# Optimization experiments

Measured on AMD Instinct MI355X. Metric: run time of the kernel, lower is better.

The kernel has to match this reference:

```python
import jax, jax.numpy as jnp
import numpy as np

N, T, F_IN, H, D_FF, C_OUT = 4096, 60, 64, 128, 256, 1


def _gru_layer(x_tnf, W_ih, W_hh, b_ih, b_hh):
    # torch nn.GRU single layer; x_tnf: [T, N, in]
    def step(h, xt):
        gi = xt @ W_ih.T + b_ih          # [N, 3H]
        gh = h @ W_hh.T + b_hh
        i_r, i_z, i_n = jnp.split(gi, 3, axis=-1)
        h_r, h_z, h_n = jnp.split(gh, 3, axis=-1)
        r = jax.nn.sigmoid(i_r + h_r)
        z = jax.nn.sigmoid(i_z + h_z)
        n = jnp.tanh(i_n + r * h_n)
        h = (1.0 - z) * n + z * h
        return h, h
    h0 = jnp.zeros((x_tnf.shape[1], W_hh.shape[1]), x_tnf.dtype)
    hT, ys = jax.lax.scan(step, h0, x_tnf)
    return hT, ys


def setup_inputs() -> dict:
    key = jax.random.key(0)
    ks = jax.random.split(key, 20)
    s_in = 1.0 / np.sqrt(F_IN)
    s_h = 1.0 / np.sqrt(H)
    inp = {
        'x': jax.random.normal(ks[0], (N, T, F_IN), jnp.float32),
        'W_ih0': jax.random.normal(ks[1], (3 * H, F_IN), jnp.float32) * s_in,
        'W_hh0': jax.random.normal(ks[2], (3 * H, H), jnp.float32) * s_h,
        'b_ih0': jax.random.normal(ks[3], (3 * H,), jnp.float32) * s_h,
        'b_hh0': jax.random.normal(ks[4], (3 * H,), jnp.float32) * s_h,
        'W_ih1': jax.random.normal(ks[5], (3 * H, H), jnp.float32) * s_h,
        'W_hh1': jax.random.normal(ks[6], (3 * H, H), jnp.float32) * s_h,
        'b_ih1': jax.random.normal(ks[7], (3 * H,), jnp.float32) * s_h,
        'b_hh1': jax.random.normal(ks[8], (3 * H,), jnp.float32) * s_h,
        'Wt': jax.random.normal(ks[9], (H, H), jnp.float32) * s_h,
        'bt': jax.random.normal(ks[10], (H,), jnp.float32) * s_h,
        'a': jax.random.normal(ks[11], (2 * H, 1), jnp.float32),
        'Wfc': jax.random.normal(ks[12], (H, H), jnp.float32) * s_h,
        'bfc': jax.random.normal(ks[13], (H,), jnp.float32) * s_h,
        'Wp1': jax.random.normal(ks[14], (D_FF, H), jnp.float32) * s_h,
        'bp1': jax.random.normal(ks[15], (D_FF,), jnp.float32) * s_h,
        'Wp2': jax.random.normal(ks[16], (C_OUT, D_FF), jnp.float32) * (1.0 / np.sqrt(D_FF)),
        'bp2': jax.random.normal(ks[17], (C_OUT,), jnp.float32) * (1.0 / np.sqrt(D_FF)),
    }
    return inp


def reference(x, W_ih0, W_hh0, b_ih0, b_hh0, W_ih1, W_hh1, b_ih1, b_hh1,
              Wt, bt, a, Wfc, bfc, Wp1, bp1, Wp2, bp2):
    x_tnf = jnp.transpose(x, (1, 0, 2))  # [T, N, F]
    _, ys0 = _gru_layer(x_tnf, W_ih0, W_hh0, b_ih0, b_hh0)
    hT, _ = _gru_layer(ys0, W_ih1, W_hh1, b_ih1, b_hh1)
    hidden = hT  # out[:, -1, :], [N, H]

    # cal_attention: score[i,j] = a[:H].x_j + a[H:].x_i  (separable GAT score)
    xt = hidden @ Wt.T + bt                      # transformation(x) == transformation(y)
    a_flat = a[:, 0]
    s_j = xt @ a_flat[:H]                        # [N], contributes per-column
    s_i = xt @ a_flat[H:]                        # [N], contributes per-row
    scores = jax.nn.leaky_relu(s_i[:, None] + s_j[None, :], negative_slope=0.01)
    att = jax.nn.softmax(scores, axis=1)         # [N, N]

    hidden = att @ hidden + hidden
    hidden = jax.nn.leaky_relu(hidden @ Wfc.T + bfc, negative_slope=0.01)
    h1 = jax.nn.gelu(hidden @ Wp1.T + bp1, approximate=False)
    out = h1 @ Wp2.T + bp2                       # [N, 1]
    return jnp.squeeze(out)                      # [N]
```

## Files before the change

kernel.cpp:

```cpp
#include <hip/hip_runtime.h>
#include <cstdint>
#include <cstddef>

#define TSTEPS 60
#define NB 4096
#define HD 128

typedef __attribute__((ext_vector_type(8))) short short8;
typedef __attribute__((ext_vector_type(4))) float f32x4;

#define WS_SJ    0
#define WS_SI    16384
#define WS_HID   32768
#define WS_HTH   2129920
#define WS_HTL   3178496
#define WS_F0H   4227072
#define WS_F0L   (WS_F0H+49152)
#define WS_FR0H  (WS_F0L+49152)
#define WS_FR0L  (WS_FR0H+98304)
#define WS_FR1H  (WS_FR0L+98304)
#define WS_FR1L  (WS_FR1H+98304)
#define WS_FR2H  (WS_FR1L+98304)
#define WS_FR2L  (WS_FR2H+98304)
#define WS_BASE  (WS_FR2L+98304)
#define WS_Y0P   WS_BASE
#define WS_FULL  (WS_Y0P + 125829120ULL)


__device__ __forceinline__ float b2f(unsigned short h){ return __uint_as_float(((unsigned)h)<<16); }
__device__ __forceinline__ unsigned short f2b(float f){
  unsigned u = __float_as_uint(f);
  u = (u + 0x7FFFu + ((u>>16)&1u)) >> 16;
  return (unsigned short)u;
}
__device__ __forceinline__ float sigm(float x){ return 1.0f/(1.0f + __expf(-x)); }
__device__ __forceinline__ float tanhfast(float x){
  float xc = fminf(fmaxf(x,-15.0f),15.0f);
  float e = __expf(2.0f*xc);
  return (e-1.0f)/(e+1.0f);
}
__device__ __forceinline__ float lrelu(float x){ return x > 0.0f ? x : 0.01f*x; }
__device__ __forceinline__ float ldr1(const void* p, size_t i, int f32){
  return f32 ? ((const float*)p)[i] : b2f(((const unsigned short*)p)[i]);
}
template<bool F32>
__device__ __forceinline__ float4 ldg4c(const void* p, size_t i){
  if (F32) return *(const float4*)((const float*)p + i);
  ushort4 u = *(const ushort4*)((const unsigned short*)p + i);
  float4 f; f.x=b2f(u.x); f.y=b2f(u.y); f.z=b2f(u.z); f.w=b2f(u.w); return f;
}
__device__ __forceinline__ f32x4 f4zero(){ f32x4 v = {0.f,0.f,0.f,0.f}; return v; }
__device__ __forceinline__ void pinv(short8& v){ asm volatile("" : "+v"(v)); }

__device__ __forceinline__ void ldsbar(){
  asm volatile("s_waitcnt lgkmcnt(0)\n\ts_barrier" ::: "memory");
}

__device__ int probe_f32(const void* p, int nprobe, volatile int* s){
  if (threadIdx.x == 0) *s = 0;
  __syncthreads();
  if ((int)threadIdx.x < nprobe) {
    float v = b2f(((const unsigned short*)p)[threadIdx.x]);
    if (!(v == v) || fabsf(v) > 1e4f) *s = 1;
  }
  __syncthreads();
  int r = *s;
  __syncthreads();
  return r;
}

__global__ void diag_kernel(float* out, float code){
  int i = blockIdx.x*256 + threadIdx.x;
  if (i < 4096) out[i] = code;
}

__device__ void repack_mat(const void* src, int f32, int K, int nks,
                           unsigned short* hi, unsigned short* lo,
                           int tid, int nthr){
  int total = 384*K;
  for (int idx = tid; idx < total; idx += nthr) {
    int j = idx & 7, lane = (idx>>3)&63, t = idx>>9;
    int ks = t % nks, g = (t/nks)%3, w = t/(nks*3);
    int row = 16*(w + 8*g) + (lane & 15);
    int k   = ks*32 + ((lane>>4)<<3) + j;
    float v = f32 ? ((const float*)src)[(size_t)row*K + k]
                  : b2f(((const unsigned short*)src)[(size_t)row*K + k]);
    unsigned short h = f2b(v);
    hi[idx] = h;
    lo[idx] = f2b(v - b2f(h));
  }
}

__global__ __launch_bounds__(256) void repack_kernel(
    const void* wih0, const void* whh0, const void* wih1, const void* whh1,
    char* ws)
{
  __shared__ int sp;
  int f0 = probe_f32(wih0, 256, &sp);
  int f1 = probe_f32(whh0, 256, &sp);
  int f2 = probe_f32(wih1, 256, &sp);
  int f3 = probe_f32(whh1, 256, &sp);
  int tid  = blockIdx.x*256 + threadIdx.x;
  int nthr = gridDim.x*256;
  repack_mat(wih0, f0,  64, 2, (unsigned short*)(ws+WS_F0H),  (unsigned short*)(ws+WS_F0L),  tid, nthr);
  repack_mat(whh0, f1, 128, 4, (unsigned short*)(ws+WS_FR0H), (unsigned short*)(ws+WS_FR0L), tid, nthr);
  repack_mat(wih1, f2, 128, 4, (unsigned short*)(ws+WS_FR1H), (unsigned short*)(ws+WS_FR1L), tid, nthr);
  repack_mat(whh1, f3, 128, 4, (unsigned short*)(ws+WS_FR2H), (unsigned short*)(ws+WS_FR2L), tid, nthr);
}

#define MFMA __builtin_amdgcn_mfma_f32_16x16x32_bf16

__global__ __launch_bounds__(1024)
void gru0_kernel(const void* __restrict__ xg,
                 const void* __restrict__ bih0, const void* __restrict__ bhh0,
                 const char* __restrict__ ws, unsigned* __restrict__ y0p)
{
  __shared__ __align__(16) unsigned short xbh[2][1152], xbl[2][1152];
  __shared__ __align__(16) unsigned short hbh[2][2176], hbl[2][2176];
  __shared__ __align__(16) float pex[8192];
  __shared__ int sp;
  const int tid  = threadIdx.x;
  const int W    = tid >> 6;
  const int cg   = W >> 1;
  const int kh   = W & 1;
  const int lane = tid & 63;
  const int ln   = lane & 15;
  const int kq   = lane >> 4;
  const int r0   = blockIdx.x * 16;

  int xf  = probe_f32(xg,   256, &sp);
  int fb0 = probe_f32(bih0, 256, &sp);
  int fh0 = probe_f32(bhh0, 256, &sp);

  const unsigned short* f0h  = (const unsigned short*)(ws+WS_F0H);
  const unsigned short* f0l  = (const unsigned short*)(ws+WS_F0L);
  const unsigned short* fr0h = (const unsigned short*)(ws+WS_FR0H);
  const unsigned short* fr0l = (const unsigned short*)(ws+WS_FR0L);

  short8 X0h[3], X0l[3];
  #pragma unroll
  for (int g = 0; g < 3; ++g) {
    int fi = (cg*3+g)*2 + kh;
    X0h[g] = *(const short8*)&f0h[fi*512 + lane*8];
    X0l[g] = *(const short8*)&f0l[fi*512 + lane*8];
    pinv(X0h[g]); pinv(X0l[g]);
  }
  short8 R0h[3][2], R0l[3][2];
  #pragma unroll
  for (int g = 0; g < 3; ++g)
    #pragma unroll
    for (int jj = 0; jj < 2; ++jj) {
      int fi = (cg*3+g)*4 + kh*2 + jj;
      R0h[g][jj] = *(const short8*)&fr0h[fi*512 + lane*8];
      R0l[g][jj] = *(const short8*)&fr0l[fi*512 + lane*8];
      pinv(R0h[g][jj]); pinv(R0l[g][jj]);
    }

  const int nr = cg*16 + ln;
  float brc0 = ldr1(bih0,nr,fb0)     + ldr1(bhh0,nr,fh0);
  float bzc0 = ldr1(bih0,nr+128,fb0) + ldr1(bhh0,nr+128,fh0);
  float bin0 = ldr1(bih0,nr+256,fb0);
  float bhn0 = ldr1(bhh0,nr+256,fh0);

  for (int i = tid; i < 2176; i += 1024) { hbh[0][i] = 0; hbl[0][i] = 0; }
  const int xm = tid >> 5, xfc = (tid & 31)*2;
  if (tid < 512) {
    size_t base = ((size_t)(r0+xm)*TSTEPS + 0)*64 + xfc;
    float v0, v1;
    if (xf) { float2 xv = *(const float2*)((const float*)xg + base); v0 = xv.x; v1 = xv.y; }
    else { ushort2 u = *(const ushort2*)((const unsigned short*)xg + base); v0 = b2f(u.x); v1 = b2f(u.y); }
    unsigned short a0 = f2b(v0), a1 = f2b(v1);
    unsigned short l0 = f2b(v0-b2f(a0)), l1 = f2b(v1-b2f(a1));
    *(unsigned*)&xbh[0][xm*72+xfc] = (unsigned)a0 | ((unsigned)a1<<16);
    *(unsigned*)&xbl[0][xm*72+xfc] = (unsigned)l0 | ((unsigned)l1<<16);
  }
  float h0o[2] = {0.f, 0.f};
  __syncthreads();

  #pragma unroll 1
  for (int t = 0; t < TSTEPS; ++t) {
    const int b0 = t & 1, b1 = b0 ^ 1;
    float v0 = 0.f, v1 = 0.f;
    const bool stg = (tid < 512) && (t+1 < TSTEPS);
    if (stg) {
      size_t base = ((size_t)(r0+xm)*TSTEPS + (t+1))*64 + xfc;
      if (xf) { float2 xv = *(const float2*)((const float*)xg + base); v0 = xv.x; v1 = xv.y; }
      else { ushort2 u = *(const ushort2*)((const unsigned short*)xg + base); v0 = b2f(u.x); v1 = b2f(u.y); }
    }

    f32x4 acc[4];
    #pragma unroll
    for (int g = 0; g < 4; ++g) acc[g] = f4zero();
    {
      short8 axh = *(const short8*)&xbh[b0][ln*72 + kh*32 + kq*8];
      short8 axl = *(const short8*)&xbl[b0][ln*72 + kh*32 + kq*8];
      #pragma unroll
      for (int g = 0; g < 3; ++g) {
        acc[g] = MFMA(axh, X0h[g], acc[g], 0,0,0);
        acc[g] = MFMA(axh, X0l[g], acc[g], 0,0,0);
        acc[g] = MFMA(axl, X0h[g], acc[g], 0,0,0);
      }
    }
    #pragma unroll
    for (int jj = 0; jj < 2; ++jj) {
      short8 ahh = *(const short8*)&hbh[b0][ln*136 + (kh*2+jj)*32 + kq*8];
      short8 ahl = *(const short8*)&hbl[b0][ln*136 + (kh*2+jj)*32 + kq*8];
      #pragma unroll
      for (int g = 0; g < 3; ++g) {
        int tgt = (g==2) ? 3 : g;
        acc[tgt] = MFMA(ahh, R0h[g][jj], acc[tgt], 0,0,0);
        acc[tgt] = MFMA(ahh, R0l[g][jj], acc[tgt], 0,0,0);
        acc[tgt] = MFMA(ahl, R0h[g][jj], acc[tgt], 0,0,0);
      }
    }

    {
      int wbase = W*512 + lane*2;
      if (kh == 0) {
        #pragma unroll
        for (int g = 0; g < 4; ++g) {
          float2 wv; wv.x = acc[g][2]; wv.y = acc[g][3];
          *(float2*)&pex[wbase + g*128] = wv;
        }
      } else {
        #pragma unroll
        for (int g = 0; g < 4; ++g) {
          float2 wv; wv.x = acc[g][0]; wv.y = acc[g][1];
          *(float2*)&pex[wbase + g*128] = wv;
        }
      }
    }
    ldsbar();

    float c0[2], c1[2], c2[2], c3[2];
    {
      int pbase = (W^1)*512 + lane*2;
      float2 p0 = *(const float2*)&pex[pbase];
      float2 p1 = *(const float2*)&pex[pbase + 128];
      float2 p2 = *(const float2*)&pex[pbase + 256];
      float2 p3 = *(const float2*)&pex[pbase + 384];
      if (kh == 0) {
        c0[0]=acc[0][0]+p0.x; c0[1]=acc[0][1]+p0.y;
        c1[0]=acc[1][0]+p1.x; c1[1]=acc[1][1]+p1.y;
        c2[0]=acc[2][0]+p2.x; c2[1]=acc[2][1]+p2.y;
        c3[0]=acc[3][0]+p3.x; c3[1]=acc[3][1]+p3.y;
      } else {
        c0[0]=acc[0][2]+p0.x; c0[1]=acc[0][3]+p0.y;
        c1[0]=acc[1][2]+p1.x; c1[1]=acc[1][3]+p1.y;
        c2[0]=acc[2][2]+p2.x; c2[1]=acc[2][3]+p2.y;
        c3[0]=acc[3][2]+p3.x; c3[1]=acc[3][3]+p3.y;
      }
    }

    unsigned short nh2[2], nl2[2];
    #pragma unroll
    for (int j = 0; j < 2; ++j) {
      float r  = sigm(c0[j] + brc0);
      float z  = sigm(c1[j] + bzc0);
      float nn = tanhfast(c2[j] + bin0 + r*(c3[j] + bhn0));
      float h  = nn + z*(h0o[j] - nn);
      h0o[j] = h;
      unsigned short hh = f2b(h);
      nh2[j] = hh; nl2[j] = f2b(h - b2f(hh));
    }
    const int rowb = kq*4 + kh*2;
    {
      size_t ybase = ((size_t)blockIdx.x*TSTEPS + t)*2048;
      #pragma unroll
      for (int j = 0; j < 2; ++j)
        y0p[ybase + (rowb+j)*128 + cg*16 + ln] =
            (unsigned)nh2[j] | ((unsigned)nl2[j] << 16);
    }
    #pragma unroll
    for (int j = 0; j < 2; ++j) {
      int off = (rowb+j)*136 + cg*16 + ln;
      hbh[b1][off] = nh2[j]; hbl[b1][off] = nl2[j];
    }
    if (stg) {
      unsigned short a0 = f2b(v0), a1 = f2b(v1);
      unsigned short l0 = f2b(v0-b2f(a0)), l1 = f2b(v1-b2f(a1));
      *(unsigned*)&xbh[b1][xm*72+xfc] = (unsigned)a0 | ((unsigned)a1<<16);
      *(unsigned*)&xbl[b1][xm*72+xfc] = (unsigned)l0 | ((unsigned)l1<<16);
    }
    ldsbar();
  }
}

__global__ __launch_bounds__(512) __attribute__((amdgpu_waves_per_eu(2,2)))
void gru1_kernel(const void* __restrict__ bih1, const void* __restrict__ bhh1,
                 const char* __restrict__ ws, const unsigned* __restrict__ y0p,
                 float* __restrict__ hidg,
                 unsigned short* __restrict__ hTh, unsigned short* __restrict__ hTl)
{
  __shared__ __align__(16) unsigned short wih1hL[49152];
  __shared__ __align__(16) unsigned short ybh[2][2176], ybl[2][2176];
  __shared__ __align__(16) unsigned short h1bh[2][2176], h1bl[2][2176];
  __shared__ int sp;
  const int tid  = threadIdx.x;
  const int w    = tid >> 6;
  const int lane = tid & 63;
  const int ln   = lane & 15;
  const int kq   = lane >> 4;
  const int r0   = blockIdx.x * 16;

  int fb1 = probe_f32(bih1, 256, &sp);
  int fh1 = probe_f32(bhh1, 256, &sp);

  const unsigned short* fr1h = (const unsigned short*)(ws+WS_FR1H);
  const unsigned short* fr1l = (const unsigned short*)(ws+WS_FR1L);
  const unsigned short* fr2h = (const unsigned short*)(ws+WS_FR2H);
  const unsigned short* fr2l = (const unsigned short*)(ws+WS_FR2L);

  for (int i = tid*8; i < 49152; i += 4096) {
    *(ushort4*)&wih1hL[i]   = *(const ushort4*)&fr1h[i];
    *(ushort4*)&wih1hL[i+4] = *(const ushort4*)&fr1h[i+4];
  }

  short8 W1hp[2][4];
  #pragma unroll
  for (int g = 0; g < 2; ++g)
    #pragma unroll
    for (int ks = 0; ks < 4; ++ks) {
      W1hp[g][ks] = *(const short8*)&fr1h[((w*3+g)*4+ks)*512 + lane*8];
      pinv(W1hp[g][ks]);
    }

  short8 W1l[3][4], R2h[3][4], R2l[3][4];
  #pragma unroll
  for (int g = 0; g < 3; ++g)
    #pragma unroll
    for (int ks = 0; ks < 4; ++ks) {
      int fi = (w*3+g)*4 + ks;
      W1l[g][ks] = *(const short8*)&fr1l[fi*512 + lane*8];
      R2h[g][ks] = *(const short8*)&fr2h[fi*512 + lane*8];
      R2l[g][ks] = *(const short8*)&fr2l[fi*512 + lane*8];
      pinv(W1l[g][ks]); pinv(R2h[g][ks]); pinv(R2l[g][ks]);
    }

  const int nr = 16*w + ln;
  float brc1 = ldr1(bih1,nr,fb1)     + ldr1(bhh1,nr,fh1);
  float bzc1 = ldr1(bih1,nr+128,fb1) + ldr1(bhh1,nr+128,fh1);
  float bin1 = ldr1(bih1,nr+256,fb1);
  float bhn1 = ldr1(bhh1,nr+256,fh1);

  for (int i = tid; i < 2176; i += 512) { h1bh[0][i] = 0; h1bl[0][i] = 0; }
  const int yi4 = tid*4, yrow = yi4 >> 7, ycol = yi4 & 127;
  {
    uint4 pv = *(const uint4*)&y0p[((size_t)blockIdx.x*TSTEPS + 0)*2048 + yi4];
    ushort4 vh, vl;
    vh.x=(unsigned short)(pv.x&0xffff); vl.x=(unsigned short)(pv.x>>16);
    vh.y=(unsigned short)(pv.y&0xffff); vl.y=(unsigned short)(pv.y>>16);
    vh.z=(unsigned short)(pv.z&0xffff); vl.z=(unsigned short)(pv.z>>16);
    vh.w=(unsigned short)(pv.w&0xffff); vl.w=(unsigned short)(pv.w>>16);
    *(ushort4*)&ybh[0][yrow*136+ycol] = vh;
    *(ushort4*)&ybl[0][yrow*136+ycol] = vl;
  }
  float h1o[4] = {0.f,0.f,0.f,0.f};
  __syncthreads();

  #pragma unroll 1
  for (int t = 0; t < TSTEPS; ++t) {
    const int b0 = t & 1, b1 = b0 ^ 1;
    uint4 pv = {0,0,0,0};
    if (t+1 < TSTEPS)
      pv = *(const uint4*)&y0p[((size_t)blockIdx.x*TSTEPS + (t+1))*2048 + yi4];

    f32x4 acc[4];
    #pragma unroll
    for (int g = 0; g < 4; ++g) acc[g] = f4zero();
    #pragma unroll
    for (int ks = 0; ks < 4; ++ks) {
      short8 ayh = *(const short8*)&ybh[b0][ln*136 + ks*32 + kq*8];
      short8 ayl = *(const short8*)&ybl[b0][ln*136 + ks*32 + kq*8];
      short8 a1h = *(const short8*)&h1bh[b0][ln*136 + ks*32 + kq*8];
      short8 a1l = *(const short8*)&h1bl[b0][ln*136 + ks*32 + kq*8];
      #pragma unroll
      for (int g = 0; g < 3; ++g) {
        int tgtI = (g==2) ? 2 : g;
        int tgtH = (g==2) ? 3 : g;
        short8 bh;
        if (g < 2) bh = W1hp[g][ks];
        else       bh = *(const short8*)&wih1hL[((w*3+2)*4+ks)*512 + lane*8];
        acc[tgtI] = MFMA(ayh, bh,         acc[tgtI], 0,0,0);
        acc[tgtI] = MFMA(ayh, W1l[g][ks], acc[tgtI], 0,0,0);
        acc[tgtI] = MFMA(ayl, bh,         acc[tgtI], 0,0,0);
        acc[tgtH] = MFMA(a1h, R2h[g][ks], acc[tgtH], 0,0,0);
        acc[tgtH] = MFMA(a1h, R2l[g][ks], acc[tgtH], 0,0,0);
        acc[tgtH] = MFMA(a1l, R2h[g][ks], acc[tgtH], 0,0,0);
      }
    }
    unsigned short nh[4], nl[4];
    #pragma unroll
    for (int rg = 0; rg < 4; ++rg) {
      float r  = sigm(acc[0][rg] + brc1);
      float z  = sigm(acc[1][rg] + bzc1);
      float nn = tanhfast(acc[2][rg] + bin1 + r*(acc[3][rg] + bhn1));
      float h  = nn + z*(h1o[rg] - nn);
      h1o[rg] = h;
      unsigned short hh = f2b(h);
      nh[rg] = hh; nl[rg] = f2b(h - b2f(hh));
    }
    #pragma unroll
    for (int rg = 0; rg < 4; ++rg) {
      int off = (kq*4+rg)*136 + w*16 + ln;
      h1bh[b1][off] = nh[rg]; h1bl[b1][off] = nl[rg];
    }
    if (t+1 < TSTEPS) {
      ushort4 vh, vl;
      vh.x=(unsigned short)(pv.x&0xffff); vl.x=(unsigned short)(pv.x>>16);
      vh.y=(unsigned short)(pv.y&0xffff); vl.y=(unsigned short)(pv.y>>16);
      vh.z=(unsigned short)(pv.z&0xffff); vl.z=(unsigned short)(pv.z>>16);
      vh.w=(unsigned short)(pv.w&0xffff); vl.w=(unsigned short)(pv.w>>16);
      *(ushort4*)&ybh[b1][yrow*136+ycol] = vh;
      *(ushort4*)&ybl[b1][yrow*136+ycol] = vl;
    }
    ldsbar();
  }

  {
    int c = w*16 + ln;
    #pragma unroll
    for (int rg = 0; rg < 4; ++rg)
      hidg[(size_t)(r0 + kq*4 + rg)*HD + c] = h1o[rg];
    #pragma unroll
    for (int rg = 0; rg < 4; ++rg) {
      unsigned short hh = f2b(h1o[rg]);
      unsigned short ll = f2b(h1o[rg] - b2f(hh));
      int n   = r0 + kq*4 + rg;
      int chn = n >> 9, ksn = (n >> 5) & 15, kqn = (n >> 3) & 3, jn = n & 7;
      size_t o = ((size_t)((w*8 + chn)*16 + ksn))*512
               + (size_t)(kqn*16 + ln)*8 + jn;
      hTh[o] = hh;
      hTl[o] = ll;
    }
  }
}

__global__ __launch_bounds__(512, 1) void gru_fb_kernel(
    const void* __restrict__ xg,
    const void* __restrict__ bih0, const void* __restrict__ bhh0,
    const void* __restrict__ bih1, const void* __restrict__ bhh1,
    const char* __restrict__ ws, float* __restrict__ hidg,
    unsigned short* __restrict__ hTh, unsigned short* __restrict__ hTl)
{
  __shared__ __align__(16) unsigned short wih0L[49152];
  __shared__ __align__(16) unsigned short xhi[1152], xlo[1152];
  __shared__ __align__(16) unsigned short h0hi[2176], h0lo[2176];
  __shared__ __align__(16) unsigned short h1hi[2176], h1lo[2176];
  __shared__ int sp;
  const int tid  = threadIdx.x;
  const int w    = tid >> 6;
  const int lane = tid & 63;
  const int ln   = lane & 15;
  const int kq   = lane >> 4;
  const int r0   = blockIdx.x * 16;

  int xf  = probe_f32(xg,   256, &sp);
  int fb0 = probe_f32(bih0, 256, &sp);
  int fh0 = probe_f32(bhh0, 256, &sp);
  int fb1 = probe_f32(bih1, 256, &sp);
  int fh1 = probe_f32(bhh1, 256, &sp);

  const unsigned short* f0h  = (const unsigned short*)(ws+WS_F0H);
  const unsigned short* f0l  = (const unsigned short*)(ws+WS_F0L);
  const unsigned short* fr0h = (const unsigned short*)(ws+WS_FR0H);
  const unsigned short* fr0l = (const unsigned short*)(ws+WS_FR0L);
  const unsigned short* fr1h = (const unsigned short*)(ws+WS_FR1H);
  const unsigned short* fr1l = (const unsigned short*)(ws+WS_FR1L);
  const unsigned short* fr2h = (const unsigned short*)(ws+WS_FR2H);
  const unsigned short* fr2l = (const unsigned short*)(ws+WS_FR2L);

  for (int i = tid*8; i < 24576; i += 4096) {
    *(ushort4*)&wih0L[i]         = *(const ushort4*)&f0h[i];
    *(ushort4*)&wih0L[i+4]       = *(const ushort4*)&f0h[i+4];
    *(ushort4*)&wih0L[24576+i]   = *(const ushort4*)&f0l[i];
    *(ushort4*)&wih0L[24576+i+4] = *(const ushort4*)&f0l[i+4];
  }
  short8 R0h[3][4], R1h[3][4], R2h[3][4];
  #pragma unroll
  for (int g = 0; g < 3; ++g)
    #pragma unroll
    for (int ks = 0; ks < 4; ++ks) {
      int fi = (w*3+g)*4 + ks;
      R0h[g][ks] = *(const short8*)&fr0h[fi*512 + lane*8];
      R1h[g][ks] = *(const short8*)&fr1h[fi*512 + lane*8];
      R2h[g][ks] = *(const short8*)&fr2h[fi*512 + lane*8];
      pinv(R0h[g][ks]); pinv(R1h[g][ks]); pinv(R2h[g][ks]);
    }
  const int nr = 16*w + ln;
  float brc0 = ldr1(bih0,nr,fb0)     + ldr1(bhh0,nr,fh0);
  float bzc0 = ldr1(bih0,nr+128,fb0) + ldr1(bhh0,nr+128,fh0);
  float bin0 = ldr1(bih0,nr+256,fb0);
  float bhn0 = ldr1(bhh0,nr+256,fh0);
  float brc1 = ldr1(bih1,nr,fb1)     + ldr1(bhh1,nr,fh1);
  float bzc1 = ldr1(bih1,nr+128,fb1) + ldr1(bhh1,nr+128,fh1);
  float bin1 = ldr1(bih1,nr+256,fb1);
  float bhn1 = ldr1(bhh1,nr+256,fh1);

  for (int i = tid; i < 2176; i += 512) {
    h0hi[i] = 0; h0lo[i] = 0; h1hi[i] = 0; h1lo[i] = 0;
  }
  float h0o[4] = {0.f,0.f,0.f,0.f};
  float h1o[4] = {0.f,0.f,0.f,0.f};
  __syncthreads();

  #pragma unroll 1
  for (int t = 0; t < TSTEPS; ++t) {
    {
      int i0 = tid*2, m = i0 >> 6, f = i0 & 63;
      size_t base = ((size_t)(r0+m)*TSTEPS + t)*64 + f;
      float v0, v1;
      if (xf) { float2 xv = *(const float2*)((const float*)xg + base); v0 = xv.x; v1 = xv.y; }
      else { ushort2 u = *(const ushort2*)((const unsigned short*)xg + base); v0 = b2f(u.x); v1 = b2f(u.y); }
      unsigned short a0 = f2b(v0), a1 = f2b(v1);
      xhi[m*72+f] = a0;              xhi[m*72+f+1] = a1;
      xlo[m*72+f] = f2b(v0-b2f(a0)); xlo[m*72+f+1] = f2b(v1-b2f(a1));
    }
    __syncthreads();
    f32x4 acc[4];
    #pragma unroll
    for (int g = 0; g < 4; ++g) acc[g] = f4zero();
    #pragma unroll
    for (int ks = 0; ks < 2; ++ks) {
      short8 axh = *(const short8*)&xhi[ln*72 + ks*32 + kq*8];
      short8 axl = *(const short8*)&xlo[ln*72 + ks*32 + kq*8];
      #pragma unroll
      for (int g = 0; g < 3; ++g) {
        int fi = (w*3+g)*2 + ks;
        short8 bh = *(const short8*)&wih0L[fi*512 + lane*8];
        short8 bl = *(const short8*)&wih0L[24576 + fi*512 + lane*8];
        acc[g] = MFMA(axh, bh, acc[g], 0,0,0);
        acc[g] = MFMA(axh, bl, acc[g], 0,0,0);
        acc[g] = MFMA(axl, bh, acc[g], 0,0,0);
      }
    }
    #pragma unroll
    for (int ks = 0; ks < 4; ++ks) {
      short8 ahh = *(const short8*)&h0hi[ln*136 + ks*32 + kq*8];
      short8 ahl = *(const short8*)&h0lo[ln*136 + ks*32 + kq*8];
      #pragma unroll
      for (int g = 0; g < 3; ++g) {
        int tgt = (g==2) ? 3 : g;
        short8 bl = *(const short8*)&fr0l[((w*3+g)*4+ks)*512 + lane*8];
        acc[tgt] = MFMA(ahh, R0h[g][ks], acc[tgt], 0,0,0);
        acc[tgt] = MFMA(ahh, bl,         acc[tgt], 0,0,0);
        acc[tgt] = MFMA(ahl, R0h[g][ks], acc[tgt], 0,0,0);
      }
    }
    unsigned short nh[4], nl[4];
    #pragma unroll
    for (int rg = 0; rg < 4; ++rg) {
      float r  = sigm(acc[0][rg] + brc0);
      float z  = sigm(acc[1][rg] + bzc0);
      float nn = tanhfast(acc[2][rg] + bin0 + r*(acc[3][rg] + bhn0));
      float h  = nn + z*(h0o[rg] - nn);
      h0o[rg] = h;
      unsigned short hh = f2b(h);
      nh[rg] = hh; nl[rg] = f2b(h - b2f(hh));
    }
    __syncthreads();
    #pragma unroll
    for (int rg = 0; rg < 4; ++rg) {
      int off = (kq*4+rg)*136 + w*16 + ln;
      h0hi[off] = nh[rg]; h0lo[off] = nl[rg];
    }
    __syncthreads();
    #pragma unroll
    for (int g = 0; g < 4; ++g) acc[g] = f4zero();
    #pragma unroll
    for (int ks = 0; ks < 4; ++ks) {
      short8 ayh = *(const short8*)&h0hi[ln*136 + ks*32 + kq*8];
      short8 ayl = *(const short8*)&h0lo[ln*136 + ks*32 + kq*8];
      short8 a1h = *(const short8*)&h1hi[ln*136 + ks*32 + kq*8];
      short8 a1l = *(const short8*)&h1lo[ln*136 + ks*32 + kq*8];
      #pragma unroll
      for (int g = 0; g < 3; ++g) {
        int tgtI = (g==2) ? 2 : g;
        int tgtH = (g==2) ? 3 : g;
        short8 blI = *(const short8*)&fr1l[((w*3+g)*4+ks)*512 + lane*8];
        short8 blH = *(const short8*)&fr2l[((w*3+g)*4+ks)*512 + lane*8];
        acc[tgtI] = MFMA(ayh, R1h[g][ks], acc[tgtI], 0,0,0);
        acc[tgtI] = MFMA(ayh, blI,        acc[tgtI], 0,0,0);
        acc[tgtI] = MFMA(ayl, R1h[g][ks], acc[tgtI], 0,0,0);
        acc[tgtH] = MFMA(a1h, R2h[g][ks], acc[tgtH], 0,0,0);
        acc[tgtH] = MFMA(a1h, blH,        acc[tgtH], 0,0,0);
        acc[tgtH] = MFMA(a1l, R2h[g][ks], acc[tgtH], 0,0,0);
      }
    }
    #pragma unroll
    for (int rg = 0; rg < 4; ++rg) {
      float r  = sigm(acc[0][rg] + brc1);
      float z  = sigm(acc[1][rg] + bzc1);
      float nn = tanhfast(acc[2][rg] + bin1 + r*(acc[3][rg] + bhn1));
      float h  = nn + z*(h1o[rg] - nn);
      h1o[rg] = h;
      unsigned short hh = f2b(h);
      nh[rg] = hh; nl[rg] = f2b(h - b2f(hh));
    }
    __syncthreads();
    #pragma unroll
    for (int rg = 0; rg < 4; ++rg) {
      int off = (kq*4+rg)*136 + w*16 + ln;
      h1hi[off] = nh[rg]; h1lo[off] = nl[rg];
    }
  }
  {
    int c = w*16 + ln;
    #pragma unroll
    for (int rg = 0; rg < 4; ++rg)
      hidg[(size_t)(r0 + kq*4 + rg)*HD + c] = h1o[rg];
    #pragma unroll
    for (int rg = 0; rg < 4; ++rg) {
      unsigned short hh = f2b(h1o[rg]);
      unsigned short ll = f2b(h1o[rg] - b2f(hh));
      int n   = r0 + kq*4 + rg;
      int chn = n >> 9, ksn = (n >> 5) & 15, kqn = (n >> 3) & 3, jn = n & 7;
      size_t o = ((size_t)((w*8 + chn)*16 + ksn))*512
               + (size_t)(kqn*16 + ln)*8 + jn;
      hTh[o] = hh;
      hTl[o] = ll;
    }
  }
}

template<bool WT32>
__device__ void sprep_body(
    const float* hidg, const void* wt, const void* bt, const void* a,
    int f_bt, int f_a, float* sjg, float* sig, float* hL, float* redb)
{
  const int tid = threadIdx.x;
  const int r0  = blockIdx.x * 16;
  for (int i = tid; i < 2048; i += 256) hL[i] = hidg[(size_t)r0*128 + i];
  __syncthreads();
  const int r = tid >> 4, cg = tid & 15, c0 = cg*8;
  float sjp = 0.f, sip = 0.f;
  #pragma unroll 1
  for (int cc = 0; cc < 8; ++cc) {
    int cI = c0 + cc;
    float acc = ldr1(bt, cI, f_bt);
    #pragma unroll 4
    for (int kq = 0; kq < 32; ++kq) {
      int k = kq*4;
      float4 wv = ldg4c<WT32>(wt, (size_t)cI*128 + k);
      float4 h = *(const float4*)&hL[r*128 + k];
      acc += wv.x*h.x + wv.y*h.y + wv.z*h.z + wv.w*h.w;
    }
    sjp += acc * ldr1(a, cI, f_a);
    sip += acc * ldr1(a, cI + 128, f_a);
  }
  redb[(r*16+cg)*2]   = sjp;
  redb[(r*16+cg)*2+1] = sip;
  __syncthreads();
  if (tid < 32) {
    int r2 = tid >> 1, wh = tid & 1;
    float s = 0.f;
    for (int g = 0; g < 16; ++g) s += redb[(r2*16+g)*2 + wh];
    if (wh == 0) sjg[r0+r2] = s; else sig[r0+r2] = s;
  }
}

__global__ __launch_bounds__(256) void sprep_kernel(
    const float* hidg, const void* wt, const void* bt, const void* a,
    float* sjg, float* sig)
{
  __shared__ float hL[2048];
  __shared__ float redb[512];
  __shared__ int sp;
  int f_wt = probe_f32(wt, 256, &sp);
  int f_bt = probe_f32(bt, 128, &sp);
  int f_a  = probe_f32(a,  256, &sp);
  if (f_wt) sprep_body<true >(hidg, wt, bt, a, f_bt, f_a, sjg, sig, hL, redb);
  else      sprep_body<false>(hidg, wt, bt, a, f_bt, f_a, sjg, sig, hL, redb);
}

template<bool PW32>
__device__ void attn_body(
    const float* sjg, const float* sig, const float* hidg,
    const unsigned short* hTh, const unsigned short* hTl,
    const void* wfc, const void* bfc, const void* wp1, const void* bp1,
    const void* wp2, const void* bp2,
    int f_bfc, int f_bp1, int f_wp2, float* outg,
    float* sjs, unsigned short* Pbuf, float* Obuf, float* redm,
    float* siL, float* miL, float* Zb)
{
  const int tid = threadIdx.x;
  const int w = tid >> 6, lane = tid & 63, ln = lane & 15, kq = lane >> 4;
  const int r0 = blockIdx.x * 16;

  for (int i = tid; i < 4096; i += 512) sjs[i] = sjg[i];
  __syncthreads();
  float mx = -1e30f;
  for (int i = tid; i < 4096; i += 512) mx = fmaxf(mx, sjs[i]);
  redm[tid] = mx;
  __syncthreads();
  for (int s = 256; s > 0; s >>= 1) {
    if (tid < s) redm[tid] = fmaxf(redm[tid], redm[tid+s]);
    __syncthreads();
  }
  if (tid < 16) {
    float si = sig[r0 + tid];
    siL[tid] = si;
    miL[tid] = lrelu(si + redm[0]);
  }
  __syncthreads();

  float zp[16];
  #pragma unroll
  for (int i = 0; i < 16; ++i) zp[i] = 0.f;
  f32x4 accO = f4zero();
  const int col = w*16 + ln;

  #define GENP(CH, BASE)                                                    \
    {                                                                       \
      unsigned short* Phi_ = (BASE);                                        \
      unsigned short* Plo_ = (BASE) + 8320;                                 \
      float sjv = sjs[(CH)*512 + tid];                                      \
      _Pragma("unroll")                                                     \
      for (int i = 0; i < 16; ++i) {                                        \
        float v = lrelu(siL[i] + sjv);                                      \
        float p = __expf(v - miL[i]);                                       \
        zp[i] += p;                                                         \
        unsigned short hh = f2b(p);                                         \
        Phi_[i*520 + tid] = hh;                                             \
        Plo_[i*520 + tid] = f2b(p - b2f(hh));                               \
      }                                                                     \
    }

  GENP(0, Pbuf);
  __syncthreads();

  #pragma unroll 1
  for (int ch = 0; ch < 8; ++ch) {
    const int b = ch & 1;
    unsigned short* Phi = Pbuf + b*16640;
    unsigned short* Plo = Phi + 8320;
    #pragma unroll
    for (int ks = 0; ks < 16; ++ks) {
      short8 Ah = *(const short8*)&Phi[ln*520 + ks*32 + kq*8];
      short8 Al = *(const short8*)&Plo[ln*520 + ks*32 + kq*8];
      size_t bo = ((size_t)((w*8 + ch)*16 + ks))*512 + (size_t)lane*8;
      short8 Bh = *(const short8*)&hTh[bo];
      short8 Bl = *(const short8*)&hTl[bo];
      accO = MFMA(Ah, Bh, accO, 0,0,0);
      accO = MFMA(Ah, Bl, accO, 0,0,0);
      accO = MFMA(Al, Bh, accO, 0,0,0);
    }
    if (ch < 7) GENP(ch+1, Pbuf + (b^1)*16640);
    __syncthreads();
  }
  #undef GENP

  #pragma unroll
  for (int rg = 0; rg < 4; ++rg)
    Obuf[(kq*4+rg)*128 + col] = accO[rg];

  float* zarr = (float*)Pbuf;
  #pragma unroll
  for (int i = 0; i < 16; ++i) zarr[i*512 + tid] = zp[i];
  __syncthreads();
  {
    int row = tid >> 5, t0 = tid & 31;
    float s = 0.f;
    #pragma unroll
    for (int k = 0; k < 16; ++k) s += zarr[row*512 + t0 + 32*k];
    redm[row*32 + t0] = s;
  }
  __syncthreads();
  if (tid < 16) {
    float s = 0.f;
    for (int g = 0; g < 32; ++g) s += redm[tid*32 + g];
    Zb[tid] = s;
  }
  __syncthreads();

  {
    int e0 = tid*4, row = e0 >> 7, c = e0 & 127;
    float zi = Zb[row];
    #pragma unroll
    for (int e = 0; e < 4; ++e)
      Obuf[e0+e] = Obuf[e0+e]/zi + hidg[(size_t)(r0+row)*128 + c + e];
  }
  __syncthreads();

  float* h3f = sjs;
  {
    int o0 = tid*4, row = o0 >> 7, c = o0 & 127;
    #pragma unroll 1
    for (int e = 0; e < 4; ++e) {
      int cI = c + e;
      float acc = ldr1(bfc, cI, f_bfc);
      #pragma unroll 4
      for (int k4 = 0; k4 < 32; ++k4) {
        int k = k4*4;
        float4 wv = ldg4c<PW32>(wfc, (size_t)cI*128 + k);
        float4 h = *(const float4*)&Obuf[row*128 + k];
        acc += wv.x*h.x + wv.y*h.y + wv.z*h.z + wv.w*h.w;
      }
      h3f[row*128 + cI] = lrelu(acc);
    }
  }
  __syncthreads();

  float* h1f = (float*)Pbuf;
  {
    int o0 = tid*8, row = o0 >> 8, c = o0 & 255;
    #pragma unroll 1
    for (int e = 0; e < 8; ++e) {
      int cI = c + e;
      float acc = ldr1(bp1, cI, f_bp1);
      #pragma unroll 4
      for (int k4 = 0; k4 < 32; ++k4) {
        int k = k4*4;
        float4 wv = ldg4c<PW32>(wp1, (size_t)cI*128 + k);
        float4 h = *(const float4*)&h3f[row*128 + k];
        acc += wv.x*h.x + wv.y*h.y + wv.z*h.z + wv.w*h.w;
      }
      h1f[row*256 + cI] = 0.5f*acc*(1.0f + erff(acc*0.70710678118f));
    }
  }
  __syncthreads();

  {
    int row = tid >> 5, t0 = tid & 31;
    float s = 0.f;
    #pragma unroll
    for (int k = 0; k < 8; ++k) {
      int cI = t0 + 32*k;
      s += h1f[row*256 + cI] * ldr1(wp2, cI, f_wp2);
    }
    redm[row*32 + t0] = s;
  }
  __syncthreads();
  if (tid < 16) {
    float acc = ldr1(bp2, 0, f_bp1);
    for (int g = 0; g < 32; ++g) acc += redm[tid*32 + g];
    outg[r0 + tid] = acc;
  }
}

__global__ __launch_bounds__(512) void attn_kernel(
    const float* sjg, const float* sig, const float* hidg,
    const unsigned short* hTh, const unsigned short* hTl,
    const void* wfc, const void* bfc, const void* wp1, const void* bp1,
    const void* wp2, const void* bp2, float* outg)
{
  __shared__ float sjs[4096];
  __shared__ __align__(16) unsigned short Pbuf[33280];
  __shared__ float Obuf[2048];
  __shared__ float redm[512];
  __shared__ float siL[16], miL[16], Zb[16];
  __shared__ int sp;
  int f_wfc = probe_f32(wfc, 256, &sp);
  int f_bfc = probe_f32(bfc, 128, &sp);
  int f_bp1 = probe_f32(bp1, 256, &sp);
  int f_wp2 = probe_f32(wp2, 256, &sp);
  if (f_wfc) attn_body<true >(sjg, sig, hidg, hTh, hTl, wfc, bfc, wp1, bp1,
                              wp2, bp2, f_bfc, f_bp1, f_wp2, outg,
                              sjs, Pbuf, Obuf, redm, siL, miL, Zb);
  else       attn_body<false>(sjg, sig, hidg, hTh, hTl, wfc, bfc, wp1, bp1,
                              wp2, bp2, f_bfc, f_bp1, f_wp2, outg,
                              sjs, Pbuf, Obuf, redm, siL, miL, Zb);
}

extern "C" void kernel_launch(void* const* d_in, const int* in_sizes, int n_in,
                              void* d_out, int out_size, void* d_ws, size_t ws_size,
                              hipStream_t stream)
{
  float* out = (float*)d_out;
  const int expected[18] = {15728640,24576,49152,384,384,49152,49152,384,384,
                            16384,128,256,16384,128,32768,256,256,1};
  int bad = 0;
  if (n_in != 18 || out_size != 4096) bad = 1600;
  else for (int i = 0; i < 18; ++i) if (in_sizes[i] != expected[i]) { bad = 1600; break; }
  if (!bad && ws_size < (size_t)WS_BASE) bad = 1664;
  if (bad) { diag_kernel<<<16, 256, 0, stream>>>(out, (float)bad); return; }

  char* ws = (char*)d_ws;
  float*          sj  = (float*)(ws + WS_SJ);
  float*          si  = (float*)(ws + WS_SI);
  float*          hid = (float*)(ws + WS_HID);
  unsigned short* hTh = (unsigned short*)(ws + WS_HTH);
  unsigned short* hTl = (unsigned short*)(ws + WS_HTL);

  repack_kernel<<<256, 256, 0, stream>>>(d_in[1], d_in[2], d_in[5], d_in[6], ws);
  if (ws_size >= WS_FULL) {
    unsigned* y0p = (unsigned*)(ws + WS_Y0P);
    gru0_kernel<<<256, 1024, 0, stream>>>(d_in[0], d_in[3], d_in[4], ws, y0p);
    gru1_kernel<<<256, 512, 0, stream>>>(d_in[7], d_in[8], ws, y0p,
                                         hid, hTh, hTl);
  } else {
    gru_fb_kernel<<<256, 512, 0, stream>>>(d_in[0], d_in[3], d_in[4],
                                           d_in[7], d_in[8], ws, hid, hTh, hTl);
  }
  sprep_kernel<<<256, 256, 0, stream>>>(hid, d_in[9], d_in[10], d_in[11], sj, si);
  attn_kernel<<<256, 512, 0, stream>>>(sj, si, hid, hTh, hTl,
                                       d_in[12], d_in[13], d_in[14], d_in[15],
                                       d_in[16], d_in[17], out);
}
```

Baseline: 550.2 us.

## Split GRU layer-1 K-dimension across wave pairs with LDS partial-sum exchange

The second GRU layer kernel moves from 8 to 16 waves per block. Each pair of waves splits the K dimension of the per-step matmuls and exchanges half of its partial accumulators through a new LDS buffer, so each wave finishes two rows. Layer-0 output is now loaded directly from global memory into MFMA operand registers each step, replacing the double-buffered LDS staging. The low-precision input-weight fragments now sit in LDS while the high parts stay in registers. In exchange each step gains an extra barrier and an LDS round trip, and the global y loads are no longer prefetched a step ahead.

```diff
diff --git a/kernel.cpp b/kernel.cpp
--- a/kernel.cpp
+++ b/kernel.cpp
@@ -51,6 +51,15 @@
 }
 __device__ __forceinline__ f32x4 f4zero(){ f32x4 v = {0.f,0.f,0.f,0.f}; return v; }
 __device__ __forceinline__ void pinv(short8& v){ asm volatile("" : "+v"(v)); }
+
+__device__ __forceinline__ void unpack_y(uint4 a, uint4 b, short8& hi8, short8& lo8){
+  unsigned h[4], l[4];
+  h[0]=(a.x&0xffffu)|(a.y<<16); l[0]=(a.x>>16)|(a.y&0xffff0000u);
+  h[1]=(a.z&0xffffu)|(a.w<<16); l[1]=(a.z>>16)|(a.w&0xffff0000u);
+  h[2]=(b.x&0xffffu)|(b.y<<16); l[2]=(b.x>>16)|(b.y&0xffff0000u);
+  h[3]=(b.z&0xffffu)|(b.w<<16); l[3]=(b.z>>16)|(b.w&0xffff0000u);
+  hi8 = *(short8*)h; lo8 = *(short8*)l;
+}
 
 __device__ __forceinline__ void ldsbar(){
   asm volatile("s_waitcnt lgkmcnt(0)\n\ts_barrier" ::: "memory");
@@ -286,18 +295,20 @@
   }
 }
 
-__global__ __launch_bounds__(512) __attribute__((amdgpu_waves_per_eu(2,2)))
+__global__ __launch_bounds__(1024)
 void gru1_kernel(const void* __restrict__ bih1, const void* __restrict__ bhh1,
                  const char* __restrict__ ws, const unsigned* __restrict__ y0p,
                  float* __restrict__ hidg,
                  unsigned short* __restrict__ hTh, unsigned short* __restrict__ hTl)
 {
-  __shared__ __align__(16) unsigned short wih1hL[49152];
-  __shared__ __align__(16) unsigned short ybh[2][2176], ybl[2][2176];
+  __shared__ __align__(16) unsigned short wl1L[49152];
   __shared__ __align__(16) unsigned short h1bh[2][2176], h1bl[2][2176];
+  __shared__ __align__(16) float pex[8192];
   __shared__ int sp;
   const int tid  = threadIdx.x;
-  const int w    = tid >> 6;
+  const int W    = tid >> 6;
+  const int cg   = W >> 1;
+  const int kh   = W & 1;
   const int lane = tid & 63;
   const int ln   = lane & 15;
   const int kq   = lane >> 4;
@@ -311,124 +322,145 @@
   const unsigned short* fr2h = (const unsigned short*)(ws+WS_FR2H);
   const unsigned short* fr2l = (const unsigned short*)(ws+WS_FR2L);
 
-  for (int i = tid*8; i < 49152; i += 4096) {
-    *(ushort4*)&wih1hL[i]   = *(const ushort4*)&fr1h[i];
-    *(ushort4*)&wih1hL[i+4] = *(const ushort4*)&fr1h[i+4];
-  }
-
-  short8 W1hp[2][4];
-  #pragma unroll
-  for (int g = 0; g < 2; ++g)
-    #pragma unroll
-    for (int ks = 0; ks < 4; ++ks) {
-      W1hp[g][ks] = *(const short8*)&fr1h[((w*3+g)*4+ks)*512 + lane*8];
-      pinv(W1hp[g][ks]);
-    }
-
-  short8 W1l[3][4], R2h[3][4], R2l[3][4];
+  for (int i = tid*8; i < 49152; i += 8192) {
+    *(ushort4*)&wl1L[i]   = *(const ushort4*)&fr1l[i];
+    *(ushort4*)&wl1L[i+4] = *(const ushort4*)&fr1l[i+4];
+  }
+
+  short8 W1h[3][2], R2h[3][2], R2l[3][2];
   #pragma unroll
   for (int g = 0; g < 3; ++g)
     #pragma unroll
-    for (int ks = 0; ks < 4; ++ks) {
-      int fi = (w*3+g)*4 + ks;
-      W1l[g][ks] = *(const short8*)&fr1l[fi*512 + lane*8];
-      R2h[g][ks] = *(const short8*)&fr2h[fi*512 + lane*8];
-      R2l[g][ks] = *(const short8*)&fr2l[fi*512 + lane*8];
-      pinv(W1l[g][ks]); pinv(R2h[g][ks]); pinv(R2l[g][ks]);
-    }
-
-  const int nr = 16*w + ln;
+    for (int jj = 0; jj < 2; ++jj) {
+      int fi = (cg*3+g)*4 + kh*2 + jj;
+      W1h[g][jj] = *(const short8*)&fr1h[fi*512 + lane*8];
+      R2h[g][jj] = *(const short8*)&fr2h[fi*512 + lane*8];
+      R2l[g][jj] = *(const short8*)&fr2l[fi*512 + lane*8];
+      pinv(W1h[g][jj]); pinv(R2h[g][jj]); pinv(R2l[g][jj]);
+    }
+
+  const int nr = cg*16 + ln;
   float brc1 = ldr1(bih1,nr,fb1)     + ldr1(bhh1,nr,fh1);
   float bzc1 = ldr1(bih1,nr+128,fb1) + ldr1(bhh1,nr+128,fh1);
   float bin1 = ldr1(bih1,nr+256,fb1);
   float bhn1 = ldr1(bhh1,nr+256,fh1);
 
-  for (int i = tid; i < 2176; i += 512) { h1bh[0][i] = 0; h1bl[0][i] = 0; }
-  const int yi4 = tid*4, yrow = yi4 >> 7, ycol = yi4 & 127;
-  {
-    uint4 pv = *(const uint4*)&y0p[((size_t)blockIdx.x*TSTEPS + 0)*2048 + yi4];
-    ushort4 vh, vl;
-    vh.x=(unsigned short)(pv.x&0xffff); vl.x=(unsigned short)(pv.x>>16);
-    vh.y=(unsigned short)(pv.y&0xffff); vl.y=(unsigned short)(pv.y>>16);
-    vh.z=(unsigned short)(pv.z&0xffff); vl.z=(unsigned short)(pv.z>>16);
-    vh.w=(unsigned short)(pv.w&0xffff); vl.w=(unsigned short)(pv.w>>16);
-    *(ushort4*)&ybh[0][yrow*136+ycol] = vh;
-    *(ushort4*)&ybl[0][yrow*136+ycol] = vl;
-  }
-  float h1o[4] = {0.f,0.f,0.f,0.f};
-  __syncthreads();
+  for (int i = tid; i < 2176; i += 1024) { h1bh[0][i] = 0; h1bl[0][i] = 0; }
+  float h1o[2] = {0.f, 0.f};
+  __syncthreads();
+
+  const unsigned* ybase_p = y0p + (size_t)blockIdx.x*TSTEPS*2048
+                          + (size_t)ln*128 + kh*64 + kq*8;
 
   #pragma unroll 1
   for (int t = 0; t < TSTEPS; ++t) {
     const int b0 = t & 1, b1 = b0 ^ 1;
-    uint4 pv = {0,0,0,0};
-    if (t+1 < TSTEPS)
-      pv = *(const uint4*)&y0p[((size_t)blockIdx.x*TSTEPS + (t+1))*2048 + yi4];
+    const unsigned* yp = ybase_p + (size_t)t*2048;
+    uint4 ya0 = *(const uint4*)yp;
+    uint4 ya1 = *(const uint4*)(yp+4);
+    uint4 yb0 = *(const uint4*)(yp+32);
+    uint4 yb1 = *(const uint4*)(yp+36);
 
     f32x4 acc[4];
     #pragma unroll
     for (int g = 0; g < 4; ++g) acc[g] = f4zero();
-    #pragma unroll
-    for (int ks = 0; ks < 4; ++ks) {
-      short8 ayh = *(const short8*)&ybh[b0][ln*136 + ks*32 + kq*8];
-      short8 ayl = *(const short8*)&ybl[b0][ln*136 + ks*32 + kq*8];
-      short8 a1h = *(const short8*)&h1bh[b0][ln*136 + ks*32 + kq*8];
-      short8 a1l = *(const short8*)&h1bl[b0][ln*136 + ks*32 + kq*8];
+
+    #pragma unroll
+    for (int jj = 0; jj < 2; ++jj) {
+      short8 a1h = *(const short8*)&h1bh[b0][ln*136 + (kh*2+jj)*32 + kq*8];
+      short8 a1l = *(const short8*)&h1bl[b0][ln*136 + (kh*2+jj)*32 + kq*8];
+      #pragma unroll
+      for (int g = 0; g < 3; ++g) {
+        int tgtH = (g==2) ? 3 : g;
+        acc[tgtH] = MFMA(a1h, R2h[g][jj], acc[tgtH], 0,0,0);
+        acc[tgtH] = MFMA(a1h, R2l[g][jj], acc[tgtH], 0,0,0);
+        acc[tgtH] = MFMA(a1l, R2h[g][jj], acc[tgtH], 0,0,0);
+      }
+    }
+    #pragma unroll
+    for (int jj = 0; jj < 2; ++jj) {
+      short8 ayh, ayl;
+      if (jj == 0) unpack_y(ya0, ya1, ayh, ayl);
+      else         unpack_y(yb0, yb1, ayh, ayl);
       #pragma unroll
       for (int g = 0; g < 3; ++g) {
         int tgtI = (g==2) ? 2 : g;
-        int tgtH = (g==2) ? 3 : g;
-        short8 bh;
-        if (g < 2) bh = W1hp[g][ks];
-        else       bh = *(const short8*)&wih1hL[((w*3+2)*4+ks)*512 + lane*8];
-        acc[tgtI] = MFMA(ayh, bh,         acc[tgtI], 0,0,0);
-        acc[tgtI] = MFMA(ayh, W1l[g][ks], acc[tgtI], 0,0,0);
-        acc[tgtI] = MFMA(ayl, bh,         acc[tgtI], 0,0,0);
-        acc[tgtH] = MFMA(a1h, R2h[g][ks], acc[tgtH], 0,0,0);
-        acc[tgtH] = MFMA(a1h, R2l[g][ks], acc[tgtH], 0,0,0);
-        acc[tgtH] = MFMA(a1l, R2h[g][ks], acc[tgtH], 0,0,0);
-      }
-    }
-    unsigned short nh[4], nl[4];
-    #pragma unroll
-    for (int rg = 0; rg < 4; ++rg) {
-      float r  = sigm(acc[0][rg] + brc1);
-      float z  = sigm(acc[1][rg] + bzc1);
-      float nn = tanhfast(acc[2][rg] + bin1 + r*(acc[3][rg] + bhn1));
-      float h  = nn + z*(h1o[rg] - nn);
-      h1o[rg] = h;
+        short8 bl = *(const short8*)&wl1L[((cg*3+g)*4 + kh*2 + jj)*512 + lane*8];
+        acc[tgtI] = MFMA(ayh, W1h[g][jj], acc[tgtI], 0,0,0);
+        acc[tgtI] = MFMA(ayh, bl,         acc[tgtI], 0,0,0);
+        acc[tgtI] = MFMA(ayl, W1h[g][jj], acc[tgtI], 0,0,0);
+      }
+    }
+
+    {
+      int wbase = W*512 + lane*2;
+      if (kh == 0) {
+        #pragma unroll
+        for (int g = 0; g < 4; ++g) {
+          float2 wv; wv.x = acc[g][2]; wv.y = acc[g][3];
+          *(float2*)&pex[wbase + g*128] = wv;
+        }
+      } else {
+        #pragma unroll
+        for (int g = 0; g < 4; ++g) {
+          float2 wv; wv.x = acc[g][0]; wv.y = acc[g][1];
+          *(float2*)&pex[wbase + g*128] = wv;
+        }
+      }
+    }
+    ldsbar();
+
+    float c0[2], c1[2], c2[2], c3[2];
+    {
+      int pbase = (W^1)*512 + lane*2;
+      float2 p0 = *(const float2*)&pex[pbase];
+      float2 p1 = *(const float2*)&pex[pbase + 128];
+      float2 p2 = *(const float2*)&pex[pbase + 256];
+      float2 p3 = *(const float2*)&pex[pbase + 384];
+      if (kh == 0) {
+        c0[0]=acc[0][0]+p0.x; c0[1]=acc[0][1]+p0.y;
+        c1[0]=acc[1][0]+p1.x; c1[1]=acc[1][1]+p1.y;
+        c2[0]=acc[2][0]+p2.x; c2[1]=acc[2][1]+p2.y;
+        c3[0]=acc[3][0]+p3.x; c3[1]=acc[3][1]+p3.y;
+      } else {
+        c0[0]=acc[0][2]+p0.x; c0[1]=acc[0][3]+p0.y;
+        c1[0]=acc[1][2]+p1.x; c1[1]=acc[1][3]+p1.y;
+        c2[0]=acc[2][2]+p2.x; c2[1]=acc[2][3]+p2.y;
+        c3[0]=acc[3][2]+p3.x; c3[1]=acc[3][3]+p3.y;
+      }
+    }
+
+    unsigned short nh2[2], nl2[2];
+    #pragma unroll
+    for (int j = 0; j < 2; ++j) {
+      float r  = sigm(c0[j] + brc1);
+      float z  = sigm(c1[j] + bzc1);
+      float nn = tanhfast(c2[j] + bin1 + r*(c3[j] + bhn1));
+      float h  = nn + z*(h1o[j] - nn);
+      h1o[j] = h;
       unsigned short hh = f2b(h);
-      nh[rg] = hh; nl[rg] = f2b(h - b2f(hh));
-    }
-    #pragma unroll
-    for (int rg = 0; rg < 4; ++rg) {
-      int off = (kq*4+rg)*136 + w*16 + ln;
-      h1bh[b1][off] = nh[rg]; h1bl[b1][off] = nl[rg];
-    }
-    if (t+1 < TSTEPS) {
-      ushort4 vh, vl;
-      vh.x=(unsigned short)(pv.x&0xffff); vl.x=(unsigned short)(pv.x>>16);
-      vh.y=(unsigned short)(pv.y&0xffff); vl.y=(unsigned short)(pv.y>>16);
-      vh.z=(unsigned short)(pv.z&0xffff); vl.z=(unsigned short)(pv.z>>16);
-      vh.w=(unsigned short)(pv.w&0xffff); vl.w=(unsigned short)(pv.w>>16);
-      *(ushort4*)&ybh[b1][yrow*136+ycol] = vh;
-      *(ushort4*)&ybl[b1][yrow*136+ycol] = vl;
+      nh2[j] = hh; nl2[j] = f2b(h - b2f(hh));
+    }
+    const int rowb = kq*4 + kh*2;
+    #pragma unroll
+    for (int j = 0; j < 2; ++j) {
+      int off = (rowb+j)*136 + cg*16 + ln;
+      h1bh[b1][off] = nh2[j]; h1bl[b1][off] = nl2[j];
     }
     ldsbar();
   }
 
   {
-    int c = w*16 + ln;
-    #pragma unroll
-    for (int rg = 0; rg < 4; ++rg)
-      hidg[(size_t)(r0 + kq*4 + rg)*HD + c] = h1o[rg];
-    #pragma unroll
-    for (int rg = 0; rg < 4; ++rg) {
-      unsigned short hh = f2b(h1o[rg]);
-      unsigned short ll = f2b(h1o[rg] - b2f(hh));
-      int n   = r0 + kq*4 + rg;
+    const int rowb = kq*4 + kh*2;
+    int c = cg*16 + ln;
+    #pragma unroll
+    for (int j = 0; j < 2; ++j) {
+      int n = r0 + rowb + j;
+      hidg[(size_t)n*HD + c] = h1o[j];
+      unsigned short hh = f2b(h1o[j]);
+      unsigned short ll = f2b(h1o[j] - b2f(hh));
       int chn = n >> 9, ksn = (n >> 5) & 15, kqn = (n >> 3) & 3, jn = n & 7;
-      size_t o = ((size_t)((w*8 + chn)*16 + ksn))*512
+      size_t o = ((size_t)((cg*8 + chn)*16 + ksn))*512
                + (size_t)(kqn*16 + ln)*8 + jn;
       hTh[o] = hh;
       hTl[o] = ll;
@@ -886,8 +918,8 @@
   if (ws_size >= WS_FULL) {
     unsigned* y0p = (unsigned*)(ws + WS_Y0P);
     gru0_kernel<<<256, 1024, 0, stream>>>(d_in[0], d_in[3], d_in[4], ws, y0p);
-    gru1_kernel<<<256, 512, 0, stream>>>(d_in[7], d_in[8], ws, y0p,
-                                         hid, hTh, hTl);
+    gru1_kernel<<<256, 1024, 0, stream>>>(d_in[7], d_in[8], ws, y0p,
+                                          hid, hTh, hTl);
   } else {
     gru_fb_kernel<<<256, 512, 0, stream>>>(d_in[0], d_in[3], d_in[4],
                                            d_in[7], d_in[8], ws, hid, hTh, hTl);
```

Result: slower. 657.6 us (+19.5%).

## Precompute next-step GRU layer-1 input projection ahead of the step barrier

Applied to the files above, without the earlier changes.

Moves the layer-1 input-to-hidden MFMA work for step t+1 out of step t+1's accumulation and into the tail of step t, carried in a separate accumulator. After each barrier the serial critical path then holds only the recurrent h·W_hh MFMAs. The y staging now prefetches two steps ahead: two steps are preloaded at startup, and each iteration writes into the buffer it just finished consuming. The total MFMA count is unchanged; the cost is twelve more live accumulator registers and a longer pre-barrier section.

```diff
diff --git a/kernel.cpp b/kernel.cpp
--- a/kernel.cpp
+++ b/kernel.cpp
@@ -345,45 +345,54 @@
 
   for (int i = tid; i < 2176; i += 512) { h1bh[0][i] = 0; h1bl[0][i] = 0; }
   const int yi4 = tid*4, yrow = yi4 >> 7, ycol = yi4 & 127;
-  {
-    uint4 pv = *(const uint4*)&y0p[((size_t)blockIdx.x*TSTEPS + 0)*2048 + yi4];
+  #pragma unroll
+  for (int tt = 0; tt < 2; ++tt) {
+    uint4 pv = *(const uint4*)&y0p[((size_t)blockIdx.x*TSTEPS + tt)*2048 + yi4];
     ushort4 vh, vl;
     vh.x=(unsigned short)(pv.x&0xffff); vl.x=(unsigned short)(pv.x>>16);
     vh.y=(unsigned short)(pv.y&0xffff); vl.y=(unsigned short)(pv.y>>16);
     vh.z=(unsigned short)(pv.z&0xffff); vl.z=(unsigned short)(pv.z>>16);
     vh.w=(unsigned short)(pv.w&0xffff); vl.w=(unsigned short)(pv.w>>16);
-    *(ushort4*)&ybh[0][yrow*136+ycol] = vh;
-    *(ushort4*)&ybl[0][yrow*136+ycol] = vl;
+    *(ushort4*)&ybh[tt][yrow*136+ycol] = vh;
+    *(ushort4*)&ybl[tt][yrow*136+ycol] = vl;
   }
   float h1o[4] = {0.f,0.f,0.f,0.f};
   __syncthreads();
+
+  f32x4 accY[3];
+  #pragma unroll
+  for (int g = 0; g < 3; ++g) accY[g] = f4zero();
+  #pragma unroll
+  for (int ks = 0; ks < 4; ++ks) {
+    short8 ayh = *(const short8*)&ybh[0][ln*136 + ks*32 + kq*8];
+    short8 ayl = *(const short8*)&ybl[0][ln*136 + ks*32 + kq*8];
+    #pragma unroll
+    for (int g = 0; g < 3; ++g) {
+      short8 bh;
+      if (g < 2) bh = W1hp[g][ks];
+      else       bh = *(const short8*)&wih1hL[((w*3+2)*4+ks)*512 + lane*8];
+      accY[g] = MFMA(ayh, bh,         accY[g], 0,0,0);
+      accY[g] = MFMA(ayh, W1l[g][ks], accY[g], 0,0,0);
+      accY[g] = MFMA(ayl, bh,         accY[g], 0,0,0);
+    }
+  }
 
   #pragma unroll 1
   for (int t = 0; t < TSTEPS; ++t) {
     const int b0 = t & 1, b1 = b0 ^ 1;
     uint4 pv = {0,0,0,0};
-    if (t+1 < TSTEPS)
-      pv = *(const uint4*)&y0p[((size_t)blockIdx.x*TSTEPS + (t+1))*2048 + yi4];
+    if (t+2 < TSTEPS)
+      pv = *(const uint4*)&y0p[((size_t)blockIdx.x*TSTEPS + (t+2))*2048 + yi4];
 
     f32x4 acc[4];
-    #pragma unroll
-    for (int g = 0; g < 4; ++g) acc[g] = f4zero();
+    acc[0] = accY[0]; acc[1] = accY[1]; acc[2] = accY[2]; acc[3] = f4zero();
     #pragma unroll
     for (int ks = 0; ks < 4; ++ks) {
-      short8 ayh = *(const short8*)&ybh[b0][ln*136 + ks*32 + kq*8];
-      short8 ayl = *(const short8*)&ybl[b0][ln*136 + ks*32 + kq*8];
       short8 a1h = *(const short8*)&h1bh[b0][ln*136 + ks*32 + kq*8];
       short8 a1l = *(const short8*)&h1bl[b0][ln*136 + ks*32 + kq*8];
       #pragma unroll
       for (int g = 0; g < 3; ++g) {
-        int tgtI = (g==2) ? 2 : g;
         int tgtH = (g==2) ? 3 : g;
-        short8 bh;
-        if (g < 2) bh = W1hp[g][ks];
-        else       bh = *(const short8*)&wih1hL[((w*3+2)*4+ks)*512 + lane*8];
-        acc[tgtI] = MFMA(ayh, bh,         acc[tgtI], 0,0,0);
-        acc[tgtI] = MFMA(ayh, W1l[g][ks], acc[tgtI], 0,0,0);
-        acc[tgtI] = MFMA(ayl, bh,         acc[tgtI], 0,0,0);
         acc[tgtH] = MFMA(a1h, R2h[g][ks], acc[tgtH], 0,0,0);
         acc[tgtH] = MFMA(a1h, R2l[g][ks], acc[tgtH], 0,0,0);
         acc[tgtH] = MFMA(a1l, R2h[g][ks], acc[tgtH], 0,0,0);
@@ -405,14 +414,32 @@
       int off = (kq*4+rg)*136 + w*16 + ln;
       h1bh[b1][off] = nh[rg]; h1bl[b1][off] = nl[rg];
     }
-    if (t+1 < TSTEPS) {
+    if (t+2 < TSTEPS) {
       ushort4 vh, vl;
       vh.x=(unsigned short)(pv.x&0xffff); vl.x=(unsigned short)(pv.x>>16);
       vh.y=(unsigned short)(pv.y&0xffff); vl.y=(unsigned short)(pv.y>>16);
       vh.z=(unsigned short)(pv.z&0xffff); vl.z=(unsigned short)(pv.z>>16);
       vh.w=(unsigned short)(pv.w&0xffff); vl.w=(unsigned short)(pv.w>>16);
-      *(ushort4*)&ybh[b1][yrow*136+ycol] = vh;
-      *(ushort4*)&ybl[b1][yrow*136+ycol] = vl;
+      *(ushort4*)&ybh[b0][yrow*136+ycol] = vh;
+      *(ushort4*)&ybl[b0][yrow*136+ycol] = vl;
+    }
+    if (t+1 < TSTEPS) {
+      #pragma unroll
+      for (int g = 0; g < 3; ++g) accY[g] = f4zero();
+      #pragma unroll
+      for (int ks = 0; ks < 4; ++ks) {
+        short8 ayh = *(const short8*)&ybh[b1][ln*136 + ks*32 + kq*8];
+        short8 ayl = *(const short8*)&ybl[b1][ln*136 + ks*32 + kq*8];
+        #pragma unroll
+        for (int g = 0; g < 3; ++g) {
+          short8 bh;
+          if (g < 2) bh = W1hp[g][ks];
+          else       bh = *(const short8*)&wih1hL[((w*3+2)*4+ks)*512 + lane*8];
+          accY[g] = MFMA(ayh, bh,         accY[g], 0,0,0);
+          accY[g] = MFMA(ayh, W1l[g][ks], accY[g], 0,0,0);
+          accY[g] = MFMA(ayl, bh,         accY[g], 0,0,0);
+        }
+      }
     }
     ldsbar();
   }
```

After: 552.4 us. No clear change (+0.4%).
